# Kernel optimization log

Measured on AMD Instinct MI355X. Metric: run time of the kernel, lower is better.

Reference implementation:

```python
import jax, jax.numpy as jnp
import numpy as np

B, S, D = 4, 2048, 1024
NUM_CODES = 16384


def setup_inputs() -> dict:
    key = jax.random.key(0)
    k1, k2 = jax.random.split(key)
    inputs = jax.random.normal(k1, (B, S, D), dtype=jnp.float32)
    codebook = jax.random.normal(k2, (NUM_CODES, D), dtype=jnp.float32)
    return {"inputs": inputs, "codebook": codebook, "kcodes": 8}


def reference(inputs, codebook, kcodes):
    # logits = -cdist(inputs, codebook, p=2); squared distance is monotonic
    # with euclidean distance, so top-k indices are identical (no sqrt needed).
    x2 = jnp.sum(inputs * inputs, axis=-1, keepdims=True)        # [B,S,1]
    c2 = jnp.sum(codebook * codebook, axis=-1)                   # [C]
    xc = jnp.einsum('bsd,cd->bsc', inputs, codebook)             # [B,S,C]
    logits = -(x2 - 2.0 * xc + c2)                               # -squared dist
    _, codebook_ids = jax.lax.top_k(logits, kcodes)              # [B,S,K]
    gathered = codebook[codebook_ids]                            # [B,S,K,D]
    outputs = gathered.sum(axis=-2) / kcodes                     # [B,S,D]
    return outputs, codebook_ids
```

## Files before the change

kernel.cpp:

```cpp
#include <hip/hip_runtime.h>
#include <hip/hip_bf16.h>
#include <float.h>

#define R_TOTAL 8192
#define D_DIM   1024
#define C_TOTAL 16384
#define KSEL    8
#define XN  ((size_t)R_TOTAL * D_DIM)
#define CBN ((size_t)C_TOTAL * D_DIM)
#define NSPLIT  8
#define SEGC    (C_TOTAL / NSPLIT)
#define NCHUNK  (SEGC / 256)
#define NKT     (NCHUNK * 16)
#define NC_RES  24

typedef __attribute__((ext_vector_type(8)))  short short8v;
typedef __attribute__((ext_vector_type(16))) float f32x16;
typedef __attribute__((ext_vector_type(8)))  unsigned short ushort8;

__device__ __forceinline__ unsigned short f2bf(float f) {
  unsigned u = __float_as_uint(f);
  u = (u + 0x7fffu + ((u >> 16) & 1u)) >> 16;
  return (unsigned short)u;
}

__device__ __forceinline__ void gload_lds16(const void* g, void* l) {
  __builtin_amdgcn_global_load_lds((const __attribute__((address_space(1))) void*)g,
                                   (__attribute__((address_space(3))) void*)l, 16, 0, 0);
}

__global__ void cvt_kernel(const float* __restrict__ X, const float* __restrict__ CB,
                           unsigned short* __restrict__ Xb, unsigned short* __restrict__ CBb) {
  size_t e = ((size_t)blockIdx.x * 256 + threadIdx.x) * 8;
  const float* src; unsigned short* dst; size_t off;
  if (e < XN) { src = X;  dst = Xb;  off = e; }
  else        { src = CB; dst = CBb; off = e - XN; }
  float4 v0 = *(const float4*)(src + off);
  float4 v1 = *(const float4*)(src + off + 4);
  ushort8 o;
  o[0]=f2bf(v0.x); o[1]=f2bf(v0.y); o[2]=f2bf(v0.z); o[3]=f2bf(v0.w);
  o[4]=f2bf(v1.x); o[5]=f2bf(v1.y); o[6]=f2bf(v1.z); o[7]=f2bf(v1.w);
  *(ushort8*)(dst + off) = o;
}

__global__ void c2_kernel(const float* __restrict__ cb, float* __restrict__ c2) {
  const int wave = threadIdx.x >> 6;
  const int lane = threadIdx.x & 63;
  const int code = blockIdx.x * 4 + wave;
  const float* row = cb + (size_t)code * D_DIM;
  float s = 0.f;
  #pragma unroll
  for (int i = 0; i < D_DIM / 64; ++i) { float v = row[lane + i * 64]; s += v * v; }
  #pragma unroll
  for (int off = 32; off >= 1; off >>= 1) s += __shfl_xor(s, off, 64);
  if (lane == 0) c2[code] = s;
}

__global__ __launch_bounds__(512, 2)
void gemm_topk_kernel(const unsigned short* __restrict__ Xb,
                      const unsigned short* __restrict__ CBb,
                      const float* __restrict__ c2g,
                      float* __restrict__ pval, int* __restrict__ pid) {
  extern __shared__ char smem[];
  float* c2s = (float*)(smem + 131072);

  const int t   = threadIdx.x;
  const int wid = t >> 6, l = t & 63;
  const int wr  = wid >> 2;
  const int wc  = wid & 3;
  const int l31 = l & 31, hi = l >> 5;

  const int xt    = blockIdx.x & 31;
  const int seg   = blockIdx.x >> 5;
  const int xbase = xt * 256;
  const int cb0   = seg * SEGC;

  *(float4*)&c2s[t * 4] = *(const float4*)(c2g + cb0 + t * 4);

  const int srow = t >> 3;
  const int sswz = (((t & 7) * 16) ^ ((srow & 7) << 4)) >> 1;
  const int fswz = (l & 7) << 4;

  f32x16 acc[4][2];
  float tv[2][KSEL]; int ti[2][KSEL];
  #pragma unroll
  for (int fm = 0; fm < 4; ++fm)
    #pragma unroll
    for (int fn = 0; fn < 2; ++fn)
      #pragma unroll
      for (int r = 0; r < 16; ++r) acc[fm][fn][r] = 0.f;
  #pragma unroll
  for (int fn = 0; fn < 2; ++fn)
    #pragma unroll
    for (int q = 0; q < KSEL; ++q) { tv[fn][q] = -FLT_MAX; ti[fn][q] = 0; }

  auto STAGE_A = [&](int g) {
    const int kbase = (g & 15) * 64;
    const int arow0 = cb0 + (g >> 4) * 256;
    char* As = smem + (g & 1) * 32768;
    #pragma unroll
    for (int i = 0; i < 4; ++i)
      gload_lds16(CBb + (size_t)(arow0 + i * 64 + srow) * D_DIM + kbase + sswz,
                  As + (i * 512 + t) * 16);
  };
  auto STAGE_X = [&](int g) {
    const int kbase = (g & 15) * 64;
    char* Xs = smem + 65536 + (g & 1) * 32768;
    #pragma unroll
    for (int i = 0; i < 4; ++i)
      gload_lds16(Xb + (size_t)(xbase + i * 64 + srow) * D_DIM + kbase + sswz,
                  Xs + (i * 512 + t) * 16);
  };

  STAGE_A(0); STAGE_X(0);

  for (int g = 0; g < NKT; ++g) {
    if (g + 1 < NKT) {
      STAGE_A(g + 1);
      asm volatile("s_waitcnt vmcnt(4)" ::: "memory");
    } else {
      asm volatile("s_waitcnt vmcnt(0)" ::: "memory");
    }
    __builtin_amdgcn_s_barrier();

    const char* As = smem + (g & 1) * 32768;
    const char* Xs = smem + 65536 + (g & 1) * 32768;

    #pragma unroll
    for (int p = 0; p < 4; ++p) {
      short8v av[4], bv[2];
      const int kb = (p * 32 + hi * 16) ^ fswz;
      #pragma unroll
      for (int fm = 0; fm < 4; ++fm)
        av[fm] = *(const short8v*)(As + (wr * 128 + fm * 32 + l31) * 128 + kb);
      #pragma unroll
      for (int fn = 0; fn < 2; ++fn)
        bv[fn] = *(const short8v*)(Xs + (wc * 64 + fn * 32 + l31) * 128 + kb);

      if (p == 1 && g + 1 < NKT) STAGE_X(g + 1);

      __builtin_amdgcn_s_setprio(1);
      #pragma unroll
      for (int fm = 0; fm < 4; ++fm)
        #pragma unroll
        for (int fn = 0; fn < 2; ++fn)
          acc[fm][fn] = __builtin_amdgcn_mfma_f32_32x32x16_bf16(
              av[fm], bv[fn], acc[fm][fn], 0, 0, 0);
      __builtin_amdgcn_s_setprio(0);
      __builtin_amdgcn_sched_barrier(0);
    }

    if ((g & 15) == 15) {
      const int ch = g >> 4;
      #pragma unroll
      for (int fm = 0; fm < 4; ++fm) {
        const int rloc = ch * 256 + wr * 128 + fm * 32 + hi * 4;
        const int idb  = cb0 + ch * 256 + wr * 128 + fm * 32 + hi * 4;
        #pragma unroll
        for (int q = 0; q < 4; ++q) {
          const float4 cq = *(const float4*)&c2s[rloc + q * 8];
          #pragma unroll
          for (int fn = 0; fn < 2; ++fn) {
            #pragma unroll
            for (int r = 0; r < 4; ++r) {
              const float c2v = (r == 0) ? cq.x : (r == 1) ? cq.y : (r == 2) ? cq.z : cq.w;
              const float s = 2.f * acc[fm][fn][q * 4 + r] - c2v;
              if (s > tv[fn][KSEL - 1]) {
                float cv = s; int ci = idb + q * 8 + r;
                #pragma unroll
                for (int q2 = 0; q2 < KSEL; ++q2) {
                  if (cv > tv[fn][q2]) {
                    const float t0 = tv[fn][q2]; tv[fn][q2] = cv; cv = t0;
                    const int   t1 = ti[fn][q2]; ti[fn][q2] = ci; ci = t1;
                  }
                }
              }
            }
          }
        }
      }
      #pragma unroll
      for (int fm = 0; fm < 4; ++fm)
        #pragma unroll
        for (int fn = 0; fn < 2; ++fn)
          #pragma unroll
          for (int r = 0; r < 16; ++r) acc[fm][fn][r] = 0.f;
    }

    __builtin_amdgcn_s_barrier();
  }

  asm volatile("s_waitcnt vmcnt(0) lgkmcnt(0)" ::: "memory");
  __builtin_amdgcn_s_barrier();
  float* mv = (float*)smem;
  int*   mi = (int*)(smem + 32768);
  #pragma unroll
  for (int fn = 0; fn < 2; ++fn) {
    const int xrL = wc * 64 + fn * 32 + l31;
    const int li  = wr * 2 + hi;
    #pragma unroll
    for (int q = 0; q < KSEL; ++q) {
      mv[xrL * 32 + li * 8 + q] = tv[fn][q];
      mi[xrL * 32 + li * 8 + q] = ti[fn][q];
    }
  }
  __syncthreads();
  if (t < 256) {
    float bvv[KSEL]; int bii[KSEL];
    #pragma unroll
    for (int q = 0; q < KSEL; ++q) { bvv[q] = -FLT_MAX; bii[q] = 0x7fffffff; }
    for (int c = 0; c < 32; ++c) {
      float cv = mv[t * 32 + c]; int ci = mi[t * 32 + c];
      if (cv > bvv[KSEL - 1] || (cv == bvv[KSEL - 1] && ci < bii[KSEL - 1])) {
        #pragma unroll
        for (int q = 0; q < KSEL; ++q) {
          if (cv > bvv[q] || (cv == bvv[q] && ci < bii[q])) {
            const float t0 = bvv[q]; bvv[q] = cv; cv = t0;
            const int   t1 = bii[q]; bii[q] = ci; ci = t1;
          }
        }
      }
    }
    const size_t base = ((size_t)(xbase + t) * NSPLIT + seg) * KSEL;
    #pragma unroll
    for (int q = 0; q < KSEL; ++q) { pval[base + q] = bvv[q]; pid[base + q] = bii[q]; }
  }
}

__global__ __launch_bounds__(256)
void rescore_kernel(const float* __restrict__ X, const float* __restrict__ CB,
                    const float* __restrict__ c2g,
                    const float* __restrict__ pval, const int* __restrict__ pid,
                    float* __restrict__ out, float* __restrict__ out_ids, int nsplit) {
  const int row = blockIdx.x;
  const int t = threadIdx.x;
  __shared__ float xs[D_DIM];
  __shared__ int   scid[NC_RES];
  __shared__ float sv[NC_RES];
  __shared__ int   topid[KSEL];

  *(float4*)&xs[t * 4] = *(const float4*)(X + (size_t)row * D_DIM + t * 4);

  const int ncand = nsplit * KSEL;
  const int NC = NC_RES < ncand ? NC_RES : ncand;

  if (t < 64) {
    float v = -FLT_MAX; int idv = 0x7fffffff;
    if (t < ncand) {
      v   = pval[(size_t)row * ncand + t];
      idv = pid[(size_t)row * ncand + t];
    }
    for (int it = 0; it < NC; ++it) {
      float bv = v; int bid = idv;
      #pragma unroll
      for (int off = 32; off >= 1; off >>= 1) {
        float ov = __shfl_xor(bv, off, 64);
        int   oi = __shfl_xor(bid, off, 64);
        if (ov > bv || (ov == bv && oi < bid)) { bv = ov; bid = oi; }
      }
      if (t == 0) scid[it] = bid;
      if (idv == bid) v = -FLT_MAX;
    }
  }
  __syncthreads();

  const int w = t >> 6, ln = t & 63;
  for (int c = w; c < NC; c += 4) {
    const int id = scid[c];
    const float* cr = CB + (size_t)id * D_DIM;
    float s = 0.f;
    #pragma unroll
    for (int i = 0; i < 4; ++i) {
      const float4 cv = *(const float4*)(cr + ln * 4 + i * 256);
      const float4 xv = *(const float4*)&xs[ln * 4 + i * 256];
      s += cv.x * xv.x + cv.y * xv.y + cv.z * xv.z + cv.w * xv.w;
    }
    #pragma unroll
    for (int off = 32; off >= 1; off >>= 1) s += __shfl_xor(s, off, 64);
    if (ln == 0) sv[c] = 2.f * s - c2g[id];
  }
  __syncthreads();

  if (t == 0) {
    float bv[KSEL]; int bi[KSEL];
    #pragma unroll
    for (int q = 0; q < KSEL; ++q) { bv[q] = -FLT_MAX; bi[q] = 0x7fffffff; }
    for (int c = 0; c < NC; ++c) {
      float cv = sv[c]; int ci = scid[c];
      #pragma unroll
      for (int q = 0; q < KSEL; ++q) {
        if (cv > bv[q] || (cv == bv[q] && ci < bi[q])) {
          const float t0 = bv[q]; bv[q] = cv; cv = t0;
          const int   t1 = bi[q]; bi[q] = ci; ci = t1;
        }
      }
    }
    #pragma unroll
    for (int q = 0; q < KSEL; ++q) {
      topid[q] = bi[q];
      out_ids[(size_t)row * KSEL + q] = (float)bi[q];
    }
  }
  __syncthreads();

  float4 a = {0.f, 0.f, 0.f, 0.f};
  #pragma unroll
  for (int q = 0; q < KSEL; ++q) {
    const float4 cv = *(const float4*)(CB + (size_t)topid[q] * D_DIM + t * 4);
    a.x += cv.x; a.y += cv.y; a.z += cv.z; a.w += cv.w;
  }
  a.x *= 0.125f; a.y *= 0.125f; a.z *= 0.125f; a.w *= 0.125f;
  *(float4*)(out + (size_t)row * D_DIM + t * 4) = a;
}

extern "C" void kernel_launch(void* const* d_in, const int* in_sizes, int n_in,
                              void* d_out, int out_size, void* d_ws, size_t ws_size,
                              hipStream_t stream) {
  const float* X  = (const float*)d_in[0];
  const float* CB = (const float*)d_in[1];

  float* out     = (float*)d_out;
  float* out_ids = out + XN;

  const size_t XbB  = XN * 2;
  const size_t CBbB = CBN * 2;
  const size_t c2B  = C_TOTAL * 4;
  const size_t pvB  = (size_t)R_TOTAL * NSPLIT * KSEL * 4;

  char* p = (char*)d_ws;
  unsigned short* Xb;
  unsigned short* CBb;
  if (ws_size >= XbB + CBbB + c2B + 2 * pvB) {
    Xb  = (unsigned short*)p; p += XbB;
    CBb = (unsigned short*)p; p += CBbB;
  } else {
    CBb = (unsigned short*)d_out;
    Xb  = (unsigned short*)p; p += XbB;
  }
  float* c2   = (float*)p; p += c2B;
  float* pval = (float*)p; p += pvB;
  int*   pid  = (int*)p;

  hipLaunchKernelGGL(cvt_kernel, dim3((unsigned)((XN + CBN) / 8 / 256)), dim3(256), 0, stream,
                     X, CB, Xb, CBb);
  hipLaunchKernelGGL(c2_kernel, dim3(C_TOTAL / 4), dim3(256), 0, stream, CB, c2);
  hipLaunchKernelGGL(gemm_topk_kernel, dim3(32 * NSPLIT), dim3(512), 136 * 1024, stream,
                     Xb, CBb, c2, pval, pid);
  hipLaunchKernelGGL(rescore_kernel, dim3(R_TOTAL), dim3(256), 0, stream,
                     X, CB, c2, pval, pid, out, out_ids, NSPLIT);
}
```

Before: 594.2 us.

## Switch candidate GEMM to per-row int8 quantization with int8 MFMA

Replaces the bf16 conversion and c2 kernels with one fused kernel that quantizes inputs and codebook to int8 with per-row scales and computes codebook norms. The candidate GEMM now uses int8 32x32x32 MFMA on smaller 128x128 tiles with 256-thread blocks and a remapped block order. It keeps 12 candidates per split instead of 8, and the exact fp32 rescore considers 28 candidates. This halves operand bytes and doubles MFMA throughput per instruction, at the cost of coarser approximate scores that the wider candidate set and exact rescoring are meant to absorb.

```diff
diff --git a/kernel.cpp b/kernel.cpp
--- a/kernel.cpp
+++ b/kernel.cpp
@@ -7,168 +7,185 @@
 #define C_TOTAL 16384
 #define KSEL    8
 #define XN  ((size_t)R_TOTAL * D_DIM)
-#define CBN ((size_t)C_TOTAL * D_DIM)
 #define NSPLIT  8
 #define SEGC    (C_TOTAL / NSPLIT)
-#define NCHUNK  (SEGC / 256)
+#define NCHUNK  16
 #define NKT     (NCHUNK * 16)
-#define NC_RES  24
-
-typedef __attribute__((ext_vector_type(8)))  short short8v;
-typedef __attribute__((ext_vector_type(16))) float f32x16;
-typedef __attribute__((ext_vector_type(8)))  unsigned short ushort8;
-
-__device__ __forceinline__ unsigned short f2bf(float f) {
-  unsigned u = __float_as_uint(f);
-  u = (u + 0x7fffu + ((u >> 16) & 1u)) >> 16;
-  return (unsigned short)u;
-}
+#define KEEP    12
+#define NC_RES  28
+
+typedef __attribute__((ext_vector_type(4)))  int  int4v;
+typedef __attribute__((ext_vector_type(16))) int  i32x16;
+typedef __attribute__((ext_vector_type(4)))  float f32x4;
 
 __device__ __forceinline__ void gload_lds16(const void* g, void* l) {
   __builtin_amdgcn_global_load_lds((const __attribute__((address_space(1))) void*)g,
                                    (__attribute__((address_space(3))) void*)l, 16, 0, 0);
 }
 
-__global__ void cvt_kernel(const float* __restrict__ X, const float* __restrict__ CB,
-                           unsigned short* __restrict__ Xb, unsigned short* __restrict__ CBb) {
-  size_t e = ((size_t)blockIdx.x * 256 + threadIdx.x) * 8;
-  const float* src; unsigned short* dst; size_t off;
-  if (e < XN) { src = X;  dst = Xb;  off = e; }
-  else        { src = CB; dst = CBb; off = e - XN; }
-  float4 v0 = *(const float4*)(src + off);
-  float4 v1 = *(const float4*)(src + off + 4);
-  ushort8 o;
-  o[0]=f2bf(v0.x); o[1]=f2bf(v0.y); o[2]=f2bf(v0.z); o[3]=f2bf(v0.w);
-  o[4]=f2bf(v1.x); o[5]=f2bf(v1.y); o[6]=f2bf(v1.z); o[7]=f2bf(v1.w);
-  *(ushort8*)(dst + off) = o;
-}
-
-__global__ void c2_kernel(const float* __restrict__ cb, float* __restrict__ c2) {
-  const int wave = threadIdx.x >> 6;
+__global__ __launch_bounds__(256)
+void quant_kernel(const float* __restrict__ X, const float* __restrict__ CB,
+                  signed char* __restrict__ Xq, signed char* __restrict__ CBq,
+                  float* __restrict__ sxg, float* __restrict__ scg,
+                  float* __restrict__ c2g) {
+  const int row  = blockIdx.x * 4 + (threadIdx.x >> 6);
   const int lane = threadIdx.x & 63;
-  const int code = blockIdx.x * 4 + wave;
-  const float* row = cb + (size_t)code * D_DIM;
-  float s = 0.f;
-  #pragma unroll
-  for (int i = 0; i < D_DIM / 64; ++i) { float v = row[lane + i * 64]; s += v * v; }
-  #pragma unroll
-  for (int off = 32; off >= 1; off >>= 1) s += __shfl_xor(s, off, 64);
-  if (lane == 0) c2[code] = s;
-}
-
-__global__ __launch_bounds__(512, 2)
-void gemm_topk_kernel(const unsigned short* __restrict__ Xb,
-                      const unsigned short* __restrict__ CBb,
-                      const float* __restrict__ c2g,
+  const bool isCB = row >= R_TOTAL;
+  const int rl = isCB ? row - R_TOTAL : row;
+  const float* src = (isCB ? CB : X) + (size_t)rl * D_DIM;
+  signed char* dst = (isCB ? CBq : Xq) + (size_t)rl * D_DIM;
+
+  float4 v[4];
+  float amax = 0.f, ss = 0.f;
+  #pragma unroll
+  for (int i = 0; i < 4; ++i) {
+    v[i] = *(const float4*)(src + i * 256 + lane * 4);
+    amax = fmaxf(amax, fmaxf(fmaxf(fabsf(v[i].x), fabsf(v[i].y)),
+                             fmaxf(fabsf(v[i].z), fabsf(v[i].w))));
+    ss += v[i].x * v[i].x + v[i].y * v[i].y + v[i].z * v[i].z + v[i].w * v[i].w;
+  }
+  #pragma unroll
+  for (int off = 32; off >= 1; off >>= 1) {
+    amax = fmaxf(amax, __shfl_xor(amax, off, 64));
+    ss += __shfl_xor(ss, off, 64);
+  }
+  const float qs = (amax > 0.f) ? 127.f / amax : 0.f;
+  #pragma unroll
+  for (int i = 0; i < 4; ++i) {
+    int q0 = (int)rintf(fminf(fmaxf(v[i].x * qs, -127.f), 127.f));
+    int q1 = (int)rintf(fminf(fmaxf(v[i].y * qs, -127.f), 127.f));
+    int q2 = (int)rintf(fminf(fmaxf(v[i].z * qs, -127.f), 127.f));
+    int q3 = (int)rintf(fminf(fmaxf(v[i].w * qs, -127.f), 127.f));
+    const int packed = (q0 & 255) | ((q1 & 255) << 8) | ((q2 & 255) << 16) | (q3 << 24);
+    ((int*)dst)[i * 64 + lane] = packed;
+  }
+  if (lane == 0) {
+    const float s = (amax > 0.f) ? amax / 127.f : 0.f;
+    if (isCB) { scg[rl] = s; c2g[rl] = ss; }
+    else      { sxg[rl] = s; }
+  }
+}
+
+__global__ __launch_bounds__(256, 2)
+void gemm_topk_kernel(const signed char* __restrict__ Xq,
+                      const signed char* __restrict__ CBq,
+                      const float* __restrict__ c2g, const float* __restrict__ scg,
+                      const float* __restrict__ sxg,
                       float* __restrict__ pval, int* __restrict__ pid) {
   extern __shared__ char smem[];
-  float* c2s = (float*)(smem + 131072);
+  float* c2s = (float*)(smem + 32768);
+  float* scs = (float*)(smem + 40960);
 
   const int t   = threadIdx.x;
   const int wid = t >> 6, l = t & 63;
-  const int wr  = wid >> 2;
-  const int wc  = wid & 3;
+  const int wr  = wid >> 1;
+  const int wc  = wid & 1;
   const int l31 = l & 31, hi = l >> 5;
 
-  const int xt    = blockIdx.x & 31;
-  const int seg   = blockIdx.x >> 5;
-  const int xbase = xt * 256;
+  const int bid  = (int)((blockIdx.x & 7) * 64 + (blockIdx.x >> 3));
+  const int xt   = bid & 63;
+  const int seg  = bid >> 6;
+  const int xbase = xt * 128;
   const int cb0   = seg * SEGC;
 
-  *(float4*)&c2s[t * 4] = *(const float4*)(c2g + cb0 + t * 4);
-
-  const int srow = t >> 3;
-  const int sswz = (((t & 7) * 16) ^ ((srow & 7) << 4)) >> 1;
-  const int fswz = (l & 7) << 4;
-
-  f32x16 acc[4][2];
-  float tv[2][KSEL]; int ti[2][KSEL];
-  #pragma unroll
-  for (int fm = 0; fm < 4; ++fm)
+  #pragma unroll
+  for (int j = 0; j < 2; ++j) {
+    const int idx = (j * 256 + t) * 4;
+    *(float4*)&c2s[idx] = *(const float4*)(c2g + cb0 + idx);
+    *(float4*)&scs[idx] = *(const float4*)(scg + cb0 + idx);
+  }
+  float fx2[2];
+  #pragma unroll
+  for (int fn = 0; fn < 2; ++fn)
+    fx2[fn] = 2.f * sxg[xbase + wc * 64 + fn * 32 + l31];
+  asm volatile("" :: "v"(fx2[0]), "v"(fx2[1]));
+
+  const int srow = t >> 2;
+  const int scol = ((t & 3) * 16) ^ ((srow & 3) << 4);
+
+  i32x16 acc[2][2];
+  float tv[2][KEEP]; int ti[2][KEEP];
+  #pragma unroll
+  for (int fm = 0; fm < 2; ++fm)
     #pragma unroll
     for (int fn = 0; fn < 2; ++fn)
       #pragma unroll
-      for (int r = 0; r < 16; ++r) acc[fm][fn][r] = 0.f;
+      for (int r = 0; r < 16; ++r) acc[fm][fn][r] = 0;
   #pragma unroll
   for (int fn = 0; fn < 2; ++fn)
     #pragma unroll
-    for (int q = 0; q < KSEL; ++q) { tv[fn][q] = -FLT_MAX; ti[fn][q] = 0; }
+    for (int q = 0; q < KEEP; ++q) { tv[fn][q] = -FLT_MAX; ti[fn][q] = 0; }
 
   auto STAGE_A = [&](int g) {
     const int kbase = (g & 15) * 64;
-    const int arow0 = cb0 + (g >> 4) * 256;
-    char* As = smem + (g & 1) * 32768;
-    #pragma unroll
-    for (int i = 0; i < 4; ++i)
-      gload_lds16(CBb + (size_t)(arow0 + i * 64 + srow) * D_DIM + kbase + sswz,
-                  As + (i * 512 + t) * 16);
+    const int arow0 = cb0 + (g >> 4) * 128;
+    char* dst = smem + (g & 1) * 8192;
+    #pragma unroll
+    for (int i = 0; i < 2; ++i)
+      gload_lds16(CBq + (size_t)(arow0 + i * 64 + srow) * D_DIM + kbase + scol,
+                  dst + i * 4096 + t * 16);
   };
   auto STAGE_X = [&](int g) {
     const int kbase = (g & 15) * 64;
-    char* Xs = smem + 65536 + (g & 1) * 32768;
-    #pragma unroll
-    for (int i = 0; i < 4; ++i)
-      gload_lds16(Xb + (size_t)(xbase + i * 64 + srow) * D_DIM + kbase + sswz,
-                  Xs + (i * 512 + t) * 16);
+    char* dst = smem + 16384 + (g & 1) * 8192;
+    #pragma unroll
+    for (int i = 0; i < 2; ++i)
+      gload_lds16(Xq + (size_t)(xbase + i * 64 + srow) * D_DIM + kbase + scol,
+                  dst + i * 4096 + t * 16);
   };
 
   STAGE_A(0); STAGE_X(0);
 
+  const int rsw = (l31 & 3) << 4;
+
   for (int g = 0; g < NKT; ++g) {
-    if (g + 1 < NKT) {
+    const char* Ab = smem + (g & 1) * 8192;
+    const char* Xb = smem + 16384 + (g & 1) * 8192;
+    const bool more = (g + 1 < NKT);
+
+    if (more) {
       STAGE_A(g + 1);
-      asm volatile("s_waitcnt vmcnt(4)" ::: "memory");
+      asm volatile("s_waitcnt vmcnt(2)" ::: "memory");
     } else {
       asm volatile("s_waitcnt vmcnt(0)" ::: "memory");
     }
     __builtin_amdgcn_s_barrier();
 
-    const char* As = smem + (g & 1) * 32768;
-    const char* Xs = smem + 65536 + (g & 1) * 32768;
-
-    #pragma unroll
-    for (int p = 0; p < 4; ++p) {
-      short8v av[4], bv[2];
-      const int kb = (p * 32 + hi * 16) ^ fswz;
-      #pragma unroll
-      for (int fm = 0; fm < 4; ++fm)
-        av[fm] = *(const short8v*)(As + (wr * 128 + fm * 32 + l31) * 128 + kb);
-      #pragma unroll
-      for (int fn = 0; fn < 2; ++fn)
-        bv[fn] = *(const short8v*)(Xs + (wc * 64 + fn * 32 + l31) * 128 + kb);
-
-      if (p == 1 && g + 1 < NKT) STAGE_X(g + 1);
-
+    #pragma unroll
+    for (int p = 0; p < 2; ++p) {
+      const int kb = (p * 32 + hi * 16) ^ rsw;
+      int4v a0 = *(const int4v*)(Ab + (wr * 64 +      l31) * 64 + kb);
+      int4v a1 = *(const int4v*)(Ab + (wr * 64 + 32 + l31) * 64 + kb);
+      int4v b0 = *(const int4v*)(Xb + (wc * 64 +      l31) * 64 + kb);
+      int4v b1 = *(const int4v*)(Xb + (wc * 64 + 32 + l31) * 64 + kb);
+      if (p == 1 && more) STAGE_X(g + 1);
       __builtin_amdgcn_s_setprio(1);
-      #pragma unroll
-      for (int fm = 0; fm < 4; ++fm)
-        #pragma unroll
-        for (int fn = 0; fn < 2; ++fn)
-          acc[fm][fn] = __builtin_amdgcn_mfma_f32_32x32x16_bf16(
-              av[fm], bv[fn], acc[fm][fn], 0, 0, 0);
+      acc[0][0] = __builtin_amdgcn_mfma_i32_32x32x32_i8(a0, b0, acc[0][0], 0, 0, 0);
+      acc[0][1] = __builtin_amdgcn_mfma_i32_32x32x32_i8(a0, b1, acc[0][1], 0, 0, 0);
+      acc[1][0] = __builtin_amdgcn_mfma_i32_32x32x32_i8(a1, b0, acc[1][0], 0, 0, 0);
+      acc[1][1] = __builtin_amdgcn_mfma_i32_32x32x32_i8(a1, b1, acc[1][1], 0, 0, 0);
       __builtin_amdgcn_s_setprio(0);
-      __builtin_amdgcn_sched_barrier(0);
     }
 
     if ((g & 15) == 15) {
       const int ch = g >> 4;
       #pragma unroll
-      for (int fm = 0; fm < 4; ++fm) {
-        const int rloc = ch * 256 + wr * 128 + fm * 32 + hi * 4;
-        const int idb  = cb0 + ch * 256 + wr * 128 + fm * 32 + hi * 4;
+      for (int fm = 0; fm < 2; ++fm) {
         #pragma unroll
         for (int q = 0; q < 4; ++q) {
-          const float4 cq = *(const float4*)&c2s[rloc + q * 8];
+          const int rloc = ch * 128 + wr * 64 + fm * 32 + q * 8 + hi * 4;
+          const f32x4 cq = *(const f32x4*)&c2s[rloc];
+          const f32x4 sq = *(const f32x4*)&scs[rloc];
           #pragma unroll
           for (int fn = 0; fn < 2; ++fn) {
             #pragma unroll
             for (int r = 0; r < 4; ++r) {
-              const float c2v = (r == 0) ? cq.x : (r == 1) ? cq.y : (r == 2) ? cq.z : cq.w;
-              const float s = 2.f * acc[fm][fn][q * 4 + r] - c2v;
-              if (s > tv[fn][KSEL - 1]) {
-                float cv = s; int ci = idb + q * 8 + r;
+              const float d = (float)acc[fm][fn][q * 4 + r];
+              const float s = fx2[fn] * sq[r] * d - cq[r];
+              if (s > tv[fn][KEEP - 1]) {
+                float cv = s; int ci = cb0 + rloc + r;
                 #pragma unroll
-                for (int q2 = 0; q2 < KSEL; ++q2) {
+                for (int q2 = 0; q2 < KEEP; ++q2) {
                   if (cv > tv[fn][q2]) {
                     const float t0 = tv[fn][q2]; tv[fn][q2] = cv; cv = t0;
                     const int   t1 = ti[fn][q2]; ti[fn][q2] = ci; ci = t1;
@@ -180,11 +197,11 @@
         }
       }
       #pragma unroll
-      for (int fm = 0; fm < 4; ++fm)
+      for (int fm = 0; fm < 2; ++fm)
         #pragma unroll
         for (int fn = 0; fn < 2; ++fn)
           #pragma unroll
-          for (int r = 0; r < 16; ++r) acc[fm][fn][r] = 0.f;
+          for (int r = 0; r < 16; ++r) acc[fm][fn][r] = 0;
     }
 
     __builtin_amdgcn_s_barrier();
@@ -193,27 +210,27 @@
   asm volatile("s_waitcnt vmcnt(0) lgkmcnt(0)" ::: "memory");
   __builtin_amdgcn_s_barrier();
   float* mv = (float*)smem;
-  int*   mi = (int*)(smem + 32768);
+  int*   mi = (int*)(smem + 25088);
   #pragma unroll
   for (int fn = 0; fn < 2; ++fn) {
     const int xrL = wc * 64 + fn * 32 + l31;
     const int li  = wr * 2 + hi;
     #pragma unroll
-    for (int q = 0; q < KSEL; ++q) {
-      mv[xrL * 32 + li * 8 + q] = tv[fn][q];
-      mi[xrL * 32 + li * 8 + q] = ti[fn][q];
+    for (int q = 0; q < KEEP; ++q) {
+      mv[xrL * 49 + li * KEEP + q] = tv[fn][q];
+      mi[xrL * 49 + li * KEEP + q] = ti[fn][q];
     }
   }
   __syncthreads();
-  if (t < 256) {
-    float bvv[KSEL]; int bii[KSEL];
-    #pragma unroll
-    for (int q = 0; q < KSEL; ++q) { bvv[q] = -FLT_MAX; bii[q] = 0x7fffffff; }
-    for (int c = 0; c < 32; ++c) {
-      float cv = mv[t * 32 + c]; int ci = mi[t * 32 + c];
-      if (cv > bvv[KSEL - 1] || (cv == bvv[KSEL - 1] && ci < bii[KSEL - 1])) {
+  if (t < 128) {
+    float bvv[KEEP]; int bii[KEEP];
+    #pragma unroll
+    for (int q = 0; q < KEEP; ++q) { bvv[q] = -FLT_MAX; bii[q] = 0x7fffffff; }
+    for (int c = 0; c < 4 * KEEP; ++c) {
+      float cv = mv[t * 49 + c]; int ci = mi[t * 49 + c];
+      if (cv > bvv[KEEP - 1] || (cv == bvv[KEEP - 1] && ci < bii[KEEP - 1])) {
         #pragma unroll
-        for (int q = 0; q < KSEL; ++q) {
+        for (int q = 0; q < KEEP; ++q) {
           if (cv > bvv[q] || (cv == bvv[q] && ci < bii[q])) {
             const float t0 = bvv[q]; bvv[q] = cv; cv = t0;
             const int   t1 = bii[q]; bii[q] = ci; ci = t1;
@@ -221,9 +238,9 @@
         }
       }
     }
-    const size_t base = ((size_t)(xbase + t) * NSPLIT + seg) * KSEL;
-    #pragma unroll
-    for (int q = 0; q < KSEL; ++q) { pval[base + q] = bvv[q]; pid[base + q] = bii[q]; }
+    const size_t base = ((size_t)(xbase + t) * NSPLIT + seg) * KEEP;
+    #pragma unroll
+    for (int q = 0; q < KEEP; ++q) { pval[base + q] = bvv[q]; pid[base + q] = bii[q]; }
   }
 }
 
@@ -231,7 +248,7 @@
 void rescore_kernel(const float* __restrict__ X, const float* __restrict__ CB,
                     const float* __restrict__ c2g,
                     const float* __restrict__ pval, const int* __restrict__ pid,
-                    float* __restrict__ out, float* __restrict__ out_ids, int nsplit) {
+                    float* __restrict__ out, float* __restrict__ out_ids) {
   const int row = blockIdx.x;
   const int t = threadIdx.x;
   __shared__ float xs[D_DIM];
@@ -241,17 +258,20 @@
 
   *(float4*)&xs[t * 4] = *(const float4*)(X + (size_t)row * D_DIM + t * 4);
 
-  const int ncand = nsplit * KSEL;
-  const int NC = NC_RES < ncand ? NC_RES : ncand;
+  const int ncand = NSPLIT * KEEP;
 
   if (t < 64) {
-    float v = -FLT_MAX; int idv = 0x7fffffff;
-    if (t < ncand) {
-      v   = pval[(size_t)row * ncand + t];
-      idv = pid[(size_t)row * ncand + t];
-    }
-    for (int it = 0; it < NC; ++it) {
-      float bv = v; int bid = idv;
+    float v0 = pval[(size_t)row * ncand + t];
+    int   i0 = pid [(size_t)row * ncand + t];
+    float v1 = -FLT_MAX; int i1 = 0x7fffffff;
+    if (t < 32) {
+      v1 = pval[(size_t)row * ncand + t + 64];
+      i1 = pid [(size_t)row * ncand + t + 64];
+    }
+    for (int it = 0; it < NC_RES; ++it) {
+      float bv; int bid;
+      if (v0 > v1 || (v0 == v1 && i0 < i1)) { bv = v0; bid = i0; }
+      else                                  { bv = v1; bid = i1; }
       #pragma unroll
       for (int off = 32; off >= 1; off >>= 1) {
         float ov = __shfl_xor(bv, off, 64);
@@ -259,13 +279,14 @@
         if (ov > bv || (ov == bv && oi < bid)) { bv = ov; bid = oi; }
       }
       if (t == 0) scid[it] = bid;
-      if (idv == bid) v = -FLT_MAX;
+      if (i0 == bid) v0 = -FLT_MAX;
+      if (i1 == bid) v1 = -FLT_MAX;
     }
   }
   __syncthreads();
 
   const int w = t >> 6, ln = t & 63;
-  for (int c = w; c < NC; c += 4) {
+  for (int c = w; c < NC_RES; c += 4) {
     const int id = scid[c];
     const float* cr = CB + (size_t)id * D_DIM;
     float s = 0.f;
@@ -285,7 +306,7 @@
     float bv[KSEL]; int bi[KSEL];
     #pragma unroll
     for (int q = 0; q < KSEL; ++q) { bv[q] = -FLT_MAX; bi[q] = 0x7fffffff; }
-    for (int c = 0; c < NC; ++c) {
+    for (int c = 0; c < NC_RES; ++c) {
       float cv = sv[c]; int ci = scid[c];
       #pragma unroll
       for (int q = 0; q < KSEL; ++q) {
@@ -322,30 +343,31 @@
   float* out     = (float*)d_out;
   float* out_ids = out + XN;
 
-  const size_t XbB  = XN * 2;
-  const size_t CBbB = CBN * 2;
+  const size_t XqB  = XN;
+  const size_t CBqB = (size_t)C_TOTAL * D_DIM;
+  const size_t sxB  = R_TOTAL * 4;
+  const size_t scB  = C_TOTAL * 4;
   const size_t c2B  = C_TOTAL * 4;
-  const size_t pvB  = (size_t)R_TOTAL * NSPLIT * KSEL * 4;
+  const size_t pvB  = (size_t)R_TOTAL * NSPLIT * KEEP * 4;
 
   char* p = (char*)d_ws;
-  unsigned short* Xb;
-  unsigned short* CBb;
-  if (ws_size >= XbB + CBbB + c2B + 2 * pvB) {
-    Xb  = (unsigned short*)p; p += XbB;
-    CBb = (unsigned short*)p; p += CBbB;
+  signed char* CBq;
+  if (ws_size >= XqB + CBqB + sxB + scB + c2B + 2 * pvB) {
+    CBq = (signed char*)p; p += CBqB;
   } else {
-    CBb = (unsigned short*)d_out;
-    Xb  = (unsigned short*)p; p += XbB;
-  }
-  float* c2   = (float*)p; p += c2B;
+    CBq = (signed char*)d_out;
+  }
+  signed char* Xq = (signed char*)p; p += XqB;
+  float* sxg  = (float*)p; p += sxB;
+  float* scg  = (float*)p; p += scB;
+  float* c2g  = (float*)p; p += c2B;
   float* pval = (float*)p; p += pvB;
   int*   pid  = (int*)p;
 
-  hipLaunchKernelGGL(cvt_kernel, dim3((unsigned)((XN + CBN) / 8 / 256)), dim3(256), 0, stream,
-                     X, CB, Xb, CBb);
-  hipLaunchKernelGGL(c2_kernel, dim3(C_TOTAL / 4), dim3(256), 0, stream, CB, c2);
-  hipLaunchKernelGGL(gemm_topk_kernel, dim3(32 * NSPLIT), dim3(512), 136 * 1024, stream,
-                     Xb, CBb, c2, pval, pid);
+  hipLaunchKernelGGL(quant_kernel, dim3((R_TOTAL + C_TOTAL) / 4), dim3(256), 0, stream,
+                     X, CB, Xq, CBq, sxg, scg, c2g);
+  hipLaunchKernelGGL(gemm_topk_kernel, dim3(64 * NSPLIT), dim3(256), 50176, stream,
+                     Xq, CBq, c2g, scg, sxg, pval, pid);
   hipLaunchKernelGGL(rescore_kernel, dim3(R_TOTAL), dim3(256), 0, stream,
-                     X, CB, c2, pval, pid, out, out_ids, NSPLIT);
-}
+                     X, CB, c2g, pval, pid, out, out_ids);
+}
```

New measurement: 680.2 us. 1.14x slower.
